# Optimization experiments

Hardware: AMD Instinct MI355X
Metric: run time of the kernel (lower is better)

The kernel has to match this reference:

```python
import jax, jax.numpy as jnp
import numpy as np

TOKENS, D_IN, FEATURES = 8192, 4096, 16384


def setup_inputs() -> dict:
    key = jax.random.key(0)
    k1, k2, k3, k4 = jax.random.split(key, 4)
    inputs = jax.random.normal(k1, (TOKENS, D_IN), dtype=jnp.float32)
    # int4-valued kernel stored as int32 (values in [0, 8) stand in for int4 codes)
    kernel = jax.random.randint(k2, (D_IN, FEATURES), 0, 8, dtype=jnp.int32)
    # per-output-channel scale; keep strictly positive to avoid div-by-zero
    scale = jax.random.uniform(k3, (1, FEATURES), dtype=jnp.float32) + 0.5
    bias = jax.random.normal(k4, (FEATURES,), dtype=jnp.float32)
    return {"inputs": inputs, "kernel": kernel, "scale": scale, "bias": bias}


def reference(inputs, kernel, scale, bias):
    # Dequantize int4 kernel: upcast + per-channel scale division, then GEMM.
    w = kernel.astype(inputs.dtype) / scale          # [D_IN, FEATURES]
    y = inputs @ w                                   # [TOKENS, FEATURES]
    return y + bias
```

## Files before the change

kernel.cpp:

```cpp
#include <hip/hip_runtime.h>

#define TOKENS 8192
#define D_IN   4096
#define FEATS  16384
#define NT     (D_IN / 128)
#define NIT    (NT / 2)

typedef __attribute__((ext_vector_type(4))) int   i4v;
typedef __attribute__((ext_vector_type(4))) float f32x4;

__device__ __forceinline__ void gload_lds16(const void* g, void* l) {
  __builtin_amdgcn_global_load_lds(
      (const __attribute__((address_space(1))) void*)g,
      (__attribute__((address_space(3))) void*)l, 16, 0, 0);
}

__device__ __forceinline__ int pack4(float4 f, float inv) {
  int a = __float2int_rn(f.x * inv), b = __float2int_rn(f.y * inv),
      c = __float2int_rn(f.z * inv), d = __float2int_rn(f.w * inv);
  return (a & 0xff) | ((b & 0xff) << 8) | ((c & 0xff) << 16) | ((d & 0xff) << 24);
}

__global__ __launch_bounds__(256) void quant_x_kernel(const float* __restrict__ x,
                                                      signed char* __restrict__ xq,
                                                      float* __restrict__ xs) {
  const int row = blockIdx.x, t = threadIdx.x;
  const float* xr = x + (long)row * D_IN;
  float4 v0 = *(const float4*)(xr + t * 16 + 0);
  float4 v1 = *(const float4*)(xr + t * 16 + 4);
  float4 v2 = *(const float4*)(xr + t * 16 + 8);
  float4 v3 = *(const float4*)(xr + t * 16 + 12);
  float m = 0.f;
  m = fmaxf(m, fmaxf(fmaxf(fabsf(v0.x), fabsf(v0.y)), fmaxf(fabsf(v0.z), fabsf(v0.w))));
  m = fmaxf(m, fmaxf(fmaxf(fabsf(v1.x), fabsf(v1.y)), fmaxf(fabsf(v1.z), fabsf(v1.w))));
  m = fmaxf(m, fmaxf(fmaxf(fabsf(v2.x), fabsf(v2.y)), fmaxf(fabsf(v2.z), fabsf(v2.w))));
  m = fmaxf(m, fmaxf(fmaxf(fabsf(v3.x), fabsf(v3.y)), fmaxf(fabsf(v3.z), fabsf(v3.w))));
#pragma unroll
  for (int off = 32; off >= 1; off >>= 1) m = fmaxf(m, __shfl_xor(m, off));
  __shared__ float wm[4];
  if ((t & 63) == 0) wm[t >> 6] = m;
  __syncthreads();
  m = fmaxf(fmaxf(wm[0], wm[1]), fmaxf(wm[2], wm[3]));
  m = fmaxf(m, 1e-20f);
  const float inv = 127.f / m;
  if (t == 0) xs[row] = m / 127.f;
  int4 o;
  o.x = pack4(v0, inv); o.y = pack4(v1, inv);
  o.z = pack4(v2, inv); o.w = pack4(v3, inv);
  *(int4*)(xq + (long)row * D_IN + t * 16) = o;
}

__global__ __launch_bounds__(256) void wtrans8_kernel(const int* __restrict__ kq,
                                                      signed char* __restrict__ wt) {
  __shared__ signed char tile[64][68];
  const int n0 = blockIdx.x * 64, k0 = blockIdx.y * 64;
  const int t = threadIdx.x;
  const int kr = t >> 4, nc = (t & 15) * 4;
#pragma unroll
  for (int p = 0; p < 4; p++) {
    int4 v = *(const int4*)(kq + (long)(k0 + kr + 16 * p) * FEATS + n0 + nc);
    tile[kr + 16 * p][nc + 0] = (signed char)v.x;
    tile[kr + 16 * p][nc + 1] = (signed char)v.y;
    tile[kr + 16 * p][nc + 2] = (signed char)v.z;
    tile[kr + 16 * p][nc + 3] = (signed char)v.w;
  }
  __syncthreads();
  const int nr = t >> 4, kc = (t & 15) * 4;
#pragma unroll
  for (int p = 0; p < 4; p++) {
    int n = nr + 16 * p;
    int o = (tile[kc + 0][n] & 0xff) | ((tile[kc + 1][n] & 0xff) << 8) |
            ((tile[kc + 2][n] & 0xff) << 16) | ((tile[kc + 3][n] & 0xff) << 24);
    *(int*)(wt + (long)(n0 + n) * D_IN + k0 + kc) = o;
  }
}

#define BAR        __builtin_amdgcn_s_barrier()
#define VMCNT0     asm volatile("s_waitcnt vmcnt(0)" ::: "memory")
#define PRIO1      __builtin_amdgcn_s_setprio(1)
#define PRIO0      __builtin_amdgcn_s_setprio(0)

#define TILEBASE(B_, MAT) (smem + (B_) * 65536 + (MAT) * 32768)

#define STAGE_A(B_, R0, KT) do { if ((KT) < NT) \
  gload_lds16(Xq + (m0 + (R0) + sr) * (long)D_IN + (long)(KT) * 128 + sgb, \
              TILEBASE(B_, 0) + (R0) * 128 + wid * 1024); } while (0)
#define STAGE_B(B_, R0, KT) do { if ((KT) < NT) \
  gload_lds16(Wq + (n0 + (R0) + sr) * (long)D_IN + (long)(KT) * 128 + sgb, \
              TILEBASE(B_, 1) + (R0) * 128 + wid * 1024); } while (0)
#define STAGE_ALL(B_, KT) do { \
  STAGE_A(B_, 0, KT); STAGE_A(B_, 64, KT); STAGE_A(B_, 128, KT); STAGE_A(B_, 192, KT); \
  STAGE_B(B_, 0, KT); STAGE_B(B_, 64, KT); STAGE_B(B_, 128, KT); STAGE_B(B_, 192, KT); } while (0)

#define LDA1(B_, I) do { \
  const char* _p = TILEBASE(B_, 0) + (wr * 128 + (I) * 16 + rl) * 128; \
  aF[(I) & 3][0] = *(const i4v*)(_p + koff0); \
  aF[(I) & 3][1] = *(const i4v*)(_p + koff1); } while (0)
#define LDA4(B_, H) do { LDA1(B_, (H)*4+0); LDA1(B_, (H)*4+1); LDA1(B_, (H)*4+2); LDA1(B_, (H)*4+3); } while (0)
#define LDB1(B_, J) do { \
  const char* _p = TILEBASE(B_, 1) + (wc * 64 + (J) * 16 + rl) * 128; \
  bF[J][0] = *(const i4v*)(_p + koff0); \
  bF[J][1] = *(const i4v*)(_p + koff1); } while (0)
#define LDB4(B_) do { LDB1(B_, 0); LDB1(B_, 1); LDB1(B_, 2); LDB1(B_, 3); } while (0)

#define MM1(I, J, KS) \
  acc[I][J] = __builtin_amdgcn_mfma_i32_16x16x64_i8(aF[(I) & 3][KS], bF[J][KS], acc[I][J], 0, 0, 0)
#define MM16(H, JH) do { \
  MM1((H)*4+0,(JH)*2+0,0); MM1((H)*4+0,(JH)*2+0,1); \
  MM1((H)*4+0,(JH)*2+1,0); MM1((H)*4+0,(JH)*2+1,1); \
  MM1((H)*4+1,(JH)*2+0,0); MM1((H)*4+1,(JH)*2+0,1); \
  MM1((H)*4+1,(JH)*2+1,0); MM1((H)*4+1,(JH)*2+1,1); \
  MM1((H)*4+2,(JH)*2+0,0); MM1((H)*4+2,(JH)*2+0,1); \
  MM1((H)*4+2,(JH)*2+1,0); MM1((H)*4+2,(JH)*2+1,1); \
  MM1((H)*4+3,(JH)*2+0,0); MM1((H)*4+3,(JH)*2+0,1); \
  MM1((H)*4+3,(JH)*2+1,0); MM1((H)*4+3,(JH)*2+1,1); } while (0)

#define KTILE(B_, TN) do { \
  LDA4(B_, 0); LDB4(B_); \
  STAGE_ALL(B_ ^ 1, TN); \
  PRIO1; MM16(0, 0); MM16(0, 1); PRIO0; \
  LDA4(B_, 1); \
  PRIO1; MM16(1, 0); MM16(1, 1); PRIO0; \
  VMCNT0; BAR; } while (0)

#define EP_PITCH 260
#define EP_HALF  (64 * EP_PITCH)

__global__ __launch_bounds__(512, 2) void gemm8i_kernel(
    const signed char* __restrict__ Xq,
    const signed char* __restrict__ Wq,
    const float* __restrict__ xs,
    const float* __restrict__ scale,
    const float* __restrict__ bias,
    float* __restrict__ C) {
  __shared__ __attribute__((aligned(16))) char smem[133120];

  const int tid = threadIdx.x;
  const int lane = tid & 63, wid = tid >> 6;
  const int wr = wid >> 2, wc = wid & 3;
  const int rl = lane & 15, q = lane >> 4;

  const int bid  = blockIdx.x;
  const int xcd  = bid & 7;
  const int l    = bid >> 3;
  const int rect = l >> 5;
  const int r    = l & 31;
  const int mloc = r & 3;
  const int nl   = r >> 2;
  const long m0 = (long)(xcd * 4 + mloc) * 256;
  const long n0 = (long)(rect * 8 + nl) * 256;

  const int sr = tid >> 3;
  const int sgb = ((tid & 7) ^ (sr & 7)) * 16;

  const int xm = (rl & 7) << 4;
  const int koff0 = (q * 16) ^ xm;
  const int koff1 = (64 + q * 16) ^ xm;

  i4v acc[8][4] = {};
  i4v aF[4][2], bF[4][2];

  STAGE_ALL(0, 0);
  VMCNT0;
  BAR;

  for (int it = 0; it < NIT; ++it) {
    KTILE(0, 2 * it + 1);
    KTILE(1, 2 * it + 2);
  }

  float rsv[4], bvv[4];
#pragma unroll
  for (int j = 0; j < 4; j++) {
    const long col = n0 + wc * 64 + j * 16 + rl;
    rsv[j] = 1.0f / scale[col];
    bvv[j] = bias[col];
  }
  float* ldsF = (float*)smem;
#pragma unroll
  for (int p = 0; p < 2; ++p) {
    if (p) BAR;
#pragma unroll
    for (int i = 0; i < 4; ++i) {
      const int ii = p * 4 + i;
      const long grow0 = m0 + wr * 128 + ii * 16 + q * 4;
#pragma unroll
      for (int r2 = 0; r2 < 4; ++r2) {
        const float xv = xs[grow0 + r2];
        const int lrow = i * 16 + q * 4 + r2;
        float* dst = ldsF + wr * EP_HALF + lrow * EP_PITCH;
#pragma unroll
        for (int j = 0; j < 4; ++j)
          dst[wc * 64 + j * 16 + rl] = (float)acc[ii][j][r2] * xv * rsv[j] + bvv[j];
      }
    }
    BAR;
#pragma unroll
    for (int h = 0; h < 2; ++h) {
      const int rr = wid * 8 + (lane >> 3);
      const long grow = m0 + h * 128 + p * 64 + rr;
      const float* src = ldsF + h * EP_HALF + rr * EP_PITCH + (lane & 7) * 4;
      float* crow = C + grow * (long)FEATS + n0 + (lane & 7) * 4;
#pragma unroll
      for (int g = 0; g < 8; ++g) {
        f32x4 v = *(const f32x4*)(src + g * 32);
        *(f32x4*)(crow + g * 32) = v;
      }
    }
  }
}

__global__ void naive_kernel(const float* __restrict__ x, const int* __restrict__ kq,
                             const float* __restrict__ scale, const float* __restrict__ bias,
                             float* __restrict__ out) {
  __shared__ float xa[16][16];
  __shared__ float wb[16][17];
  const int n = blockIdx.x * 16 + threadIdx.x;
  const int m = blockIdx.y * 16 + threadIdx.y;
  float accv = 0.f;
  for (int k0 = 0; k0 < D_IN; k0 += 16) {
    xa[threadIdx.y][threadIdx.x] = x[(long)m * D_IN + k0 + threadIdx.x];
    wb[threadIdx.y][threadIdx.x] = (float)kq[(long)(k0 + threadIdx.y) * FEATS + n];
    __syncthreads();
#pragma unroll
    for (int kk = 0; kk < 16; kk++) accv += xa[threadIdx.y][kk] * wb[kk][threadIdx.x];
    __syncthreads();
  }
  out[(long)m * FEATS + n] = accv * (1.0f / scale[n]) + bias[n];
}

extern "C" void kernel_launch(void* const* d_in, const int* in_sizes, int n_in,
                              void* d_out, int out_size, void* d_ws, size_t ws_size,
                              hipStream_t stream) {
  const float* x     = (const float*)d_in[0];
  const int*   kq    = (const int*)d_in[1];
  const float* scale = (const float*)d_in[2];
  const float* bias  = (const float*)d_in[3];
  float* out = (float*)d_out;

  const size_t need = (size_t)TOKENS * D_IN + (size_t)FEATS * D_IN + TOKENS * 4;
  if (ws_size < need) {
    naive_kernel<<<dim3(FEATS / 16, TOKENS / 16), dim3(16, 16), 0, stream>>>(
        x, kq, scale, bias, out);
    return;
  }

  signed char* Xq = (signed char*)d_ws;
  signed char* Wq = Xq + (size_t)TOKENS * D_IN;
  float* xs = (float*)(Wq + (size_t)FEATS * D_IN);

  quant_x_kernel<<<TOKENS, 256, 0, stream>>>(x, Xq, xs);
  wtrans8_kernel<<<dim3(FEATS / 64, D_IN / 64), dim3(256), 0, stream>>>(kq, Wq);
  gemm8i_kernel<<<dim3((TOKENS / 256) * (FEATS / 256)), 512, 0, stream>>>(
      Xq, Wq, xs, scale, bias, out);
}
```

Baseline: 633.8 us.

## Shrink int8 GEMM tile to 256x128 with 64-wide K steps for higher occupancy

Reworks the int8 MFMA GEMM from 256x256 tiles with 128-wide K slices to 256x128 tiles with 64-wide K slices. Each wave now owns a 64x64 output block, and LDS use drops from about 130KB to 48KB, so launch bounds allow four blocks per CU instead of two. The swizzle and epilogue are rewritten to match. The aim is more resident waves to hide latency. The cost is lower arithmetic intensity per tile, twice as many K iterations and barriers, and more global traffic for the activation tiles.

```diff
diff --git a/kernel.cpp b/kernel.cpp
--- a/kernel.cpp
+++ b/kernel.cpp
@@ -3,8 +3,7 @@
 #define TOKENS 8192
 #define D_IN   4096
 #define FEATS  16384
-#define NT     (D_IN / 128)
-#define NIT    (NT / 2)
+#define NT64   (D_IN / 64)
 
 typedef __attribute__((ext_vector_type(4))) int   i4v;
 typedef __attribute__((ext_vector_type(4))) float f32x4;
@@ -80,91 +79,74 @@
 #define PRIO1      __builtin_amdgcn_s_setprio(1)
 #define PRIO0      __builtin_amdgcn_s_setprio(0)
 
-#define TILEBASE(B_, MAT) (smem + (B_) * 65536 + (MAT) * 32768)
-
-#define STAGE_A(B_, R0, KT) do { if ((KT) < NT) \
-  gload_lds16(Xq + (m0 + (R0) + sr) * (long)D_IN + (long)(KT) * 128 + sgb, \
-              TILEBASE(B_, 0) + (R0) * 128 + wid * 1024); } while (0)
-#define STAGE_B(B_, R0, KT) do { if ((KT) < NT) \
-  gload_lds16(Wq + (n0 + (R0) + sr) * (long)D_IN + (long)(KT) * 128 + sgb, \
-              TILEBASE(B_, 1) + (R0) * 128 + wid * 1024); } while (0)
-#define STAGE_ALL(B_, KT) do { \
-  STAGE_A(B_, 0, KT); STAGE_A(B_, 64, KT); STAGE_A(B_, 128, KT); STAGE_A(B_, 192, KT); \
-  STAGE_B(B_, 0, KT); STAGE_B(B_, 64, KT); STAGE_B(B_, 128, KT); STAGE_B(B_, 192, KT); } while (0)
-
-#define LDA1(B_, I) do { \
-  const char* _p = TILEBASE(B_, 0) + (wr * 128 + (I) * 16 + rl) * 128; \
-  aF[(I) & 3][0] = *(const i4v*)(_p + koff0); \
-  aF[(I) & 3][1] = *(const i4v*)(_p + koff1); } while (0)
-#define LDA4(B_, H) do { LDA1(B_, (H)*4+0); LDA1(B_, (H)*4+1); LDA1(B_, (H)*4+2); LDA1(B_, (H)*4+3); } while (0)
-#define LDB1(B_, J) do { \
-  const char* _p = TILEBASE(B_, 1) + (wc * 64 + (J) * 16 + rl) * 128; \
-  bF[J][0] = *(const i4v*)(_p + koff0); \
-  bF[J][1] = *(const i4v*)(_p + koff1); } while (0)
-#define LDB4(B_) do { LDB1(B_, 0); LDB1(B_, 1); LDB1(B_, 2); LDB1(B_, 3); } while (0)
-
-#define MM1(I, J, KS) \
-  acc[I][J] = __builtin_amdgcn_mfma_i32_16x16x64_i8(aF[(I) & 3][KS], bF[J][KS], acc[I][J], 0, 0, 0)
-#define MM16(H, JH) do { \
-  MM1((H)*4+0,(JH)*2+0,0); MM1((H)*4+0,(JH)*2+0,1); \
-  MM1((H)*4+0,(JH)*2+1,0); MM1((H)*4+0,(JH)*2+1,1); \
-  MM1((H)*4+1,(JH)*2+0,0); MM1((H)*4+1,(JH)*2+0,1); \
-  MM1((H)*4+1,(JH)*2+1,0); MM1((H)*4+1,(JH)*2+1,1); \
-  MM1((H)*4+2,(JH)*2+0,0); MM1((H)*4+2,(JH)*2+0,1); \
-  MM1((H)*4+2,(JH)*2+1,0); MM1((H)*4+2,(JH)*2+1,1); \
-  MM1((H)*4+3,(JH)*2+0,0); MM1((H)*4+3,(JH)*2+0,1); \
-  MM1((H)*4+3,(JH)*2+1,0); MM1((H)*4+3,(JH)*2+1,1); } while (0)
+#define TILEA(B_) (smem + (B_) * 24576)
+#define TILEB(B_) (smem + (B_) * 24576 + 16384)
+
+#define STAGE_ALL(B_, KT) do { if ((KT) < NT64) { \
+  gload_lds16(Xq + aOff0 + (unsigned)(KT) * 64, TILEA(B_) + t16); \
+  gload_lds16(Xq + aOff1 + (unsigned)(KT) * 64, TILEA(B_) + 8192 + t16); \
+  gload_lds16(Wq + bOff0 + (unsigned)(KT) * 64, TILEB(B_) + t16); } } while (0)
+
+#define LDA1(B_, I) aF[I] = *(const i4v*)(TILEA(B_) + (wr * 64 + (I) * 16 + rl) * 64 + koff)
+#define LDB1(B_, J) bF[J] = *(const i4v*)(TILEB(B_) + (wc * 64 + (J) * 16 + rl) * 64 + koff)
+#define LDALL(B_) do { \
+  LDA1(B_, 0); LDA1(B_, 1); LDA1(B_, 2); LDA1(B_, 3); \
+  LDB1(B_, 0); LDB1(B_, 1); LDB1(B_, 2); LDB1(B_, 3); } while (0)
+
+#define MM16 do { \
+  _Pragma("unroll") for (int i = 0; i < 4; ++i) \
+  _Pragma("unroll") for (int j = 0; j < 4; ++j) \
+    acc[i][j] = __builtin_amdgcn_mfma_i32_16x16x64_i8(aF[i], bF[j], acc[i][j], 0, 0, 0); \
+  } while (0)
 
 #define KTILE(B_, TN) do { \
-  LDA4(B_, 0); LDB4(B_); \
   STAGE_ALL(B_ ^ 1, TN); \
-  PRIO1; MM16(0, 0); MM16(0, 1); PRIO0; \
-  LDA4(B_, 1); \
-  PRIO1; MM16(1, 0); MM16(1, 1); PRIO0; \
+  LDALL(B_); \
+  PRIO1; MM16; PRIO0; \
   VMCNT0; BAR; } while (0)
 
-#define EP_PITCH 260
-#define EP_HALF  (64 * EP_PITCH)
-
-__global__ __launch_bounds__(512, 2) void gemm8i_kernel(
+#define EP_PITCH 132
+
+__global__ __launch_bounds__(512, 4) void gemm8i_kernel(
     const signed char* __restrict__ Xq,
     const signed char* __restrict__ Wq,
     const float* __restrict__ xs,
     const float* __restrict__ scale,
     const float* __restrict__ bias,
     float* __restrict__ C) {
-  __shared__ __attribute__((aligned(16))) char smem[133120];
+  __shared__ __attribute__((aligned(16))) char smem[49152];
 
   const int tid = threadIdx.x;
   const int lane = tid & 63, wid = tid >> 6;
-  const int wr = wid >> 2, wc = wid & 3;
+  const int wr = wid >> 1, wc = wid & 1;
   const int rl = lane & 15, q = lane >> 4;
 
   const int bid  = blockIdx.x;
   const int xcd  = bid & 7;
   const int l    = bid >> 3;
-  const int rect = l >> 5;
-  const int r    = l & 31;
+  const int rect = l >> 6;
+  const int r    = l & 63;
   const int mloc = r & 3;
   const int nl   = r >> 2;
   const long m0 = (long)(xcd * 4 + mloc) * 256;
-  const long n0 = (long)(rect * 8 + nl) * 256;
-
-  const int sr = tid >> 3;
-  const int sgb = ((tid & 7) ^ (sr & 7)) * 16;
-
-  const int xm = (rl & 7) << 4;
-  const int koff0 = (q * 16) ^ xm;
-  const int koff1 = (64 + q * 16) ^ xm;
-
-  i4v acc[8][4] = {};
-  i4v aF[4][2], bF[4][2];
+  const long n0 = (long)(rect * 16 + nl) * 128;
+
+  const unsigned t16  = (unsigned)tid * 16;
+  const unsigned sgb  = (unsigned)(((tid & 3) ^ ((tid >> 3) & 3)) * 16);
+  const unsigned aOff0 = (unsigned)((m0 + (tid >> 2)) * D_IN) + sgb;
+  const unsigned aOff1 = aOff0 + 128u * D_IN;
+  const unsigned bOff0 = (unsigned)((n0 + (tid >> 2)) * D_IN) + sgb;
+
+  const int koff = ((q ^ ((rl >> 1) & 3)) << 4);
+
+  i4v acc[4][4] = {};
+  i4v aF[4], bF[4];
 
   STAGE_ALL(0, 0);
   VMCNT0;
   BAR;
 
-  for (int it = 0; it < NIT; ++it) {
+  for (int it = 0; it < NT64 / 2; ++it) {
     KTILE(0, 2 * it + 1);
     KTILE(1, 2 * it + 2);
   }
@@ -178,34 +160,30 @@
   }
   float* ldsF = (float*)smem;
 #pragma unroll
-  for (int p = 0; p < 2; ++p) {
+  for (int p = 0; p < 4; ++p) {
     if (p) BAR;
-#pragma unroll
-    for (int i = 0; i < 4; ++i) {
-      const int ii = p * 4 + i;
-      const long grow0 = m0 + wr * 128 + ii * 16 + q * 4;
-#pragma unroll
-      for (int r2 = 0; r2 < 4; ++r2) {
-        const float xv = xs[grow0 + r2];
-        const int lrow = i * 16 + q * 4 + r2;
-        float* dst = ldsF + wr * EP_HALF + lrow * EP_PITCH;
-#pragma unroll
-        for (int j = 0; j < 4; ++j)
-          dst[wc * 64 + j * 16 + rl] = (float)acc[ii][j][r2] * xv * rsv[j] + bvv[j];
+    if (wr == p) {
+#pragma unroll
+      for (int i = 0; i < 4; ++i) {
+        const long grow0 = m0 + p * 64 + i * 16 + q * 4;
+#pragma unroll
+        for (int r2 = 0; r2 < 4; ++r2) {
+          const float xv = xs[grow0 + r2];
+          float* dst = ldsF + (i * 16 + q * 4 + r2) * EP_PITCH + wc * 64;
+#pragma unroll
+          for (int j = 0; j < 4; ++j)
+            dst[j * 16 + rl] = (float)acc[i][j][r2] * xv * rsv[j] + bvv[j];
+        }
       }
     }
     BAR;
-#pragma unroll
-    for (int h = 0; h < 2; ++h) {
-      const int rr = wid * 8 + (lane >> 3);
-      const long grow = m0 + h * 128 + p * 64 + rr;
-      const float* src = ldsF + h * EP_HALF + rr * EP_PITCH + (lane & 7) * 4;
-      float* crow = C + grow * (long)FEATS + n0 + (lane & 7) * 4;
-#pragma unroll
-      for (int g = 0; g < 8; ++g) {
-        f32x4 v = *(const f32x4*)(src + g * 32);
-        *(f32x4*)(crow + g * 32) = v;
-      }
+    const int row16 = tid >> 5;
+#pragma unroll
+    for (int g = 0; g < 4; ++g) {
+      const int row = g * 16 + row16;
+      const float* src = ldsF + row * EP_PITCH + (tid & 31) * 4;
+      float* dst = C + (m0 + p * 64 + row) * (long)FEATS + n0 + (tid & 31) * 4;
+      *(f32x4*)dst = *(const f32x4*)src;
     }
   }
 }
@@ -251,6 +229,6 @@
 
   quant_x_kernel<<<TOKENS, 256, 0, stream>>>(x, Xq, xs);
   wtrans8_kernel<<<dim3(FEATS / 64, D_IN / 64), dim3(256), 0, stream>>>(kq, Wq);
-  gemm8i_kernel<<<dim3((TOKENS / 256) * (FEATS / 256)), 512, 0, stream>>>(
+  gemm8i_kernel<<<dim3((TOKENS / 256) * (FEATS / 128)), 512, 0, stream>>>(
       Xq, Wq, xs, scale, bias, out);
 }
```

New measurement: 724.5 us. 14.3% more time.
